# Kernel optimization log

Measured on AMD Instinct MI355X. Metric: run time of the kernel, lower is better.

## Reference

```python
import jax, jax.numpy as jnp
import numpy as np

EPS = 1e-8  # torch F.cosine_similarity default eps


def setup_inputs() -> dict:
    key = jax.random.key(0)
    k1, k2 = jax.random.split(key)
    xs_pad = jax.random.normal(k1, (8, 4096, 512), dtype=jnp.float32)
    spk_emb = jax.random.normal(k2, (8, 256, 512), dtype=jnp.float32)
    return {"xs_pad": xs_pad, "spk_emb": spk_emb}


def reference(xs_pad, spk_emb):
    # Faithful to F.cosine_similarity(x.unsqueeze(2), y.unsqueeze(1), dim=-1):
    #   dot(x, y) / (max(||x||, eps) * max(||y||, eps))
    # Implemented as L2-normalize then a batched GEMM -> (B, T, S), avoiding
    # the (B, T, S, D) broadcast intermediate.
    x_norm = jnp.maximum(jnp.linalg.norm(xs_pad, axis=-1, keepdims=True), EPS)
    y_norm = jnp.maximum(jnp.linalg.norm(spk_emb, axis=-1, keepdims=True), EPS)
    xn = xs_pad / x_norm          # (B, T, D)
    yn = spk_emb / y_norm         # (B, S, D)
    scores = jnp.einsum('btd,bsd->bts', xn, yn)  # (B, T, S)
    return scores
```

## Files before the change

### kernel.cpp

```cpp
#include <hip/hip_runtime.h>
#include <hip/hip_bf16.h>

#define BB 8
#define TT 4096
#define SS 256
#define DD 512

typedef __attribute__((ext_vector_type(8))) short short8;
typedef __attribute__((ext_vector_type(4))) float floatx4;
typedef __attribute__((ext_vector_type(4))) int intx4;

__device__ inline int pk2(float a, float b) {
  __hip_bfloat162 h = __float22bfloat162_rn(make_float2(a, b));
  int r;
  __builtin_memcpy(&r, &h, 4);
  return r;
}

__device__ inline short8 cvt8(float4 f0, float4 f1) {
  intx4 p;
  p[0] = pk2(f0.x, f0.y);
  p[1] = pk2(f0.z, f0.w);
  p[2] = pk2(f1.x, f1.y);
  p[3] = pk2(f1.z, f1.w);
  return __builtin_bit_cast(short8, p);
}

__global__ __launch_bounds__(256) void cos_packB_kernel(
    const float* __restrict__ spk, short* __restrict__ bp) {
  const int idx = blockIdx.x;
  const int b = idx >> 3;
  const int tn = (idx >> 2) & 1;
  const int kh = idx & 3;
  const int tid = threadIdx.x;
  short* dst = bp + (size_t)idx * 2048 * 8;
#pragma unroll
  for (int j = 0; j < 8; j++) {
    int u = j * 256 + tid;
    int row = u >> 4;
    int kblk = (u & 15) ^ (row & 15);
    const float* src =
        spk + ((size_t)(b * SS + tn * 128 + row)) * DD + kh * 128 + kblk * 8;
    float4 f0 = *(const float4*)src;
    float4 f1 = *(const float4*)(src + 4);
    short8 o = cvt8(f0, f1);
    *(short8*)(dst + (size_t)u * 8) = o;
  }
}

__global__ __launch_bounds__(256) void cos_fused_kernel(
    const float* __restrict__ xs, const short* __restrict__ bp,
    float* __restrict__ out) {
  __shared__ float sA[128 * 64];
  __shared__ short sB[128 * 128];
  __shared__ float scX[128];
  __shared__ float scY[128];

  const int tid = threadIdx.x;
  const int wave = tid >> 6;
  const int lane = tid & 63;
  const int tn = blockIdx.x;
  const int tm = blockIdx.y;
  const int b = blockIdx.z;

  const float* Abase = xs + ((size_t)b * TT + tm * 128) * DD;
  const short* Bbase = bp + ((size_t)(b * 2 + tn) * 4) * 2048 * 8;

  floatx4 acc[4][4];
#pragma unroll
  for (int i = 0; i < 4; i++)
#pragma unroll
    for (int j = 0; j < 4; j++) acc[i][j] = (floatx4){0.f, 0.f, 0.f, 0.f};
  floatx4 accG[4];
#pragma unroll
  for (int i = 0; i < 4; i++) accG[i] = (floatx4){0.f, 0.f, 0.f, 0.f};

  const int wm = wave >> 1;
  const int wn = wave & 1;
  const int quad = lane >> 4;
  const int l15 = lane & 15;
  const bool gramA = (wm == wn);

  int aoff[8];
#pragma unroll
  for (int j = 0; j < 8; j++) {
    int s = j * 256 + tid;
    int row = s >> 4;
    int blk = (s & 15) ^ (row & 15);
    aoff[j] = row * DD + blk * 4;
  }

  for (int kt = 0; kt < DD / 64; ++kt) {
    if ((kt & 1) == 0) {
      const short* gB = Bbase + (size_t)(kt >> 1) * 2048 * 8;
#pragma unroll
      for (int j = 0; j < 8; j++) {
        __builtin_amdgcn_global_load_lds(
            (const __attribute__((address_space(1))) unsigned int*)(gB +
                (size_t)(j * 256 + wave * 64 + lane) * 8),
            (__attribute__((address_space(3))) unsigned int*)(sB +
                (size_t)(j * 256 + wave * 64) * 8),
            16, 0, 0);
      }
    }
#pragma unroll
    for (int j = 0; j < 8; j++) {
      __builtin_amdgcn_global_load_lds(
          (const __attribute__((address_space(1))) unsigned int*)(Abase +
              aoff[j] + kt * 64),
          (__attribute__((address_space(3))) unsigned int*)(sA +
              (j * 256 + wave * 64) * 4),
          16, 0, 0);
    }
    __syncthreads();

#pragma unroll
    for (int ks = 0; ks < 2; ks++) {
      short8 af[4], bfr[4];
      const int b0s = ks * 8 + quad * 2;
      const int bslot = (kt & 1) * 8 + ks * 4 + quad;
#pragma unroll
      for (int im = 0; im < 4; im++) {
        int row = wm * 64 + im * 16 + l15;
        int s0 = b0s ^ (row & 15);
        int s1 = (b0s + 1) ^ (row & 15);
        float4 f0 = *(const float4*)(sA + row * 64 + s0 * 4);
        float4 f1 = *(const float4*)(sA + row * 64 + s1 * 4);
        af[im] = cvt8(f0, f1);
      }
#pragma unroll
      for (int in = 0; in < 4; in++) {
        int row = wn * 64 + in * 16 + l15;
        int s = bslot ^ (row & 15);
        bfr[in] = *(const short8*)(sB + row * 128 + s * 8);
      }
#pragma unroll
      for (int im = 0; im < 4; im++)
#pragma unroll
        for (int in = 0; in < 4; in++)
          acc[im][in] = __builtin_amdgcn_mfma_f32_16x16x32_bf16(
              af[im], bfr[in], acc[im][in], 0, 0, 0);
      if (gramA) {
#pragma unroll
        for (int im = 0; im < 4; im++)
          accG[im] = __builtin_amdgcn_mfma_f32_16x16x32_bf16(
              af[im], af[im], accG[im], 0, 0, 0);
      } else {
#pragma unroll
        for (int in = 0; in < 4; in++)
          accG[in] = __builtin_amdgcn_mfma_f32_16x16x32_bf16(
              bfr[in], bfr[in], accG[in], 0, 0, 0);
      }
    }
    __syncthreads();
  }

  if (quad == (l15 >> 2)) {
#pragma unroll
    for (int i = 0; i < 4; i++) {
      float inv = 1.0f / fmaxf(sqrtf(accG[i][l15 & 3]), 1e-8f);
      if (gramA)
        scX[wm * 64 + i * 16 + l15] = inv;
      else
        scY[wn * 64 + i * 16 + l15] = inv;
    }
  }
  __syncthreads();

  float* Obase = out + ((size_t)b * TT + tm * 128) * SS + tn * 128;
#pragma unroll
  for (int im = 0; im < 4; im++) {
#pragma unroll
    for (int in = 0; in < 4; in++) {
      int col = wn * 64 + in * 16 + l15;
      float yv = scY[col];
#pragma unroll
      for (int r = 0; r < 4; r++) {
        int row = wm * 64 + im * 16 + quad * 4 + r;
        Obase[row * SS + col] = acc[im][in][r] * scX[row] * yv;
      }
    }
  }
}

extern "C" void kernel_launch(void* const* d_in, const int* in_sizes, int n_in,
                              void* d_out, int out_size, void* d_ws,
                              size_t ws_size, hipStream_t stream) {
  const float* xs = (const float*)d_in[0];
  const float* spk = (const float*)d_in[1];
  float* out = (float*)d_out;
  short* bp = (short*)d_ws;

  hipLaunchKernelGGL(cos_packB_kernel, dim3(64), dim3(256), 0, stream, spk,
                     bp);
  hipLaunchKernelGGL(cos_fused_kernel, dim3(SS / 128, TT / 128, BB), dim3(256),
                     0, stream, xs, bp, out);
}
```

Before: 116.1 us.

## Widen output tile to full S=256 so each block reads its A rows once

Each block now covers all 256 speaker columns instead of 128. Grid shrinks from 2x32x8 to 32x8, and the B pack kernel writes a layout of 256 columns per K-quarter. This removes the duplicated fp32 A loads and the repeated bf16 conversion and gram accumulation for A, which the two N-tiles previously each did. In exchange each block needs about twice the accumulator registers and 64KB of LDS for B. The grid falls to 256 blocks, which may hurt occupancy and latency hiding.

```diff
diff --git a/kernel.cpp b/kernel.cpp
--- a/kernel.cpp
+++ b/kernel.cpp
@@ -29,18 +29,17 @@
 __global__ __launch_bounds__(256) void cos_packB_kernel(
     const float* __restrict__ spk, short* __restrict__ bp) {
   const int idx = blockIdx.x;
-  const int b = idx >> 3;
-  const int tn = (idx >> 2) & 1;
+  const int b = idx >> 2;
   const int kh = idx & 3;
   const int tid = threadIdx.x;
-  short* dst = bp + (size_t)idx * 2048 * 8;
+  short* dst = bp + (size_t)idx * 4096 * 8;
 #pragma unroll
-  for (int j = 0; j < 8; j++) {
+  for (int j = 0; j < 16; j++) {
     int u = j * 256 + tid;
-    int row = u >> 4;
-    int kblk = (u & 15) ^ (row & 15);
+    int col = u >> 4;
+    int kblk = (u & 15) ^ (col & 15);
     const float* src =
-        spk + ((size_t)(b * SS + tn * 128 + row)) * DD + kh * 128 + kblk * 8;
+        spk + ((size_t)(b * SS + col)) * DD + kh * 128 + kblk * 8;
     float4 f0 = *(const float4*)src;
     float4 f1 = *(const float4*)(src + 4);
     short8 o = cvt8(f0, f1);
@@ -52,28 +51,27 @@
     const float* __restrict__ xs, const short* __restrict__ bp,
     float* __restrict__ out) {
   __shared__ float sA[128 * 64];
-  __shared__ short sB[128 * 128];
+  __shared__ short sB[256 * 128];
   __shared__ float scX[128];
-  __shared__ float scY[128];
+  __shared__ float scY[256];
 
   const int tid = threadIdx.x;
   const int wave = tid >> 6;
   const int lane = tid & 63;
-  const int tn = blockIdx.x;
-  const int tm = blockIdx.y;
-  const int b = blockIdx.z;
+  const int tm = blockIdx.x;
+  const int b = blockIdx.y;
 
   const float* Abase = xs + ((size_t)b * TT + tm * 128) * DD;
-  const short* Bbase = bp + ((size_t)(b * 2 + tn) * 4) * 2048 * 8;
+  const short* Bregions = bp + (size_t)(b * 4) * 4096 * 8;
 
-  floatx4 acc[4][4];
+  floatx4 acc[4][8];
 #pragma unroll
   for (int i = 0; i < 4; i++)
 #pragma unroll
-    for (int j = 0; j < 4; j++) acc[i][j] = (floatx4){0.f, 0.f, 0.f, 0.f};
-  floatx4 accG[4];
+    for (int j = 0; j < 8; j++) acc[i][j] = (floatx4){0.f, 0.f, 0.f, 0.f};
+  floatx4 accG[8];
 #pragma unroll
-  for (int i = 0; i < 4; i++) accG[i] = (floatx4){0.f, 0.f, 0.f, 0.f};
+  for (int i = 0; i < 8; i++) accG[i] = (floatx4){0.f, 0.f, 0.f, 0.f};
 
   const int wm = wave >> 1;
   const int wn = wave & 1;
@@ -92,9 +90,9 @@
 
   for (int kt = 0; kt < DD / 64; ++kt) {
     if ((kt & 1) == 0) {
-      const short* gB = Bbase + (size_t)(kt >> 1) * 2048 * 8;
+      const short* gB = Bregions + (size_t)(kt >> 1) * 4096 * 8;
 #pragma unroll
-      for (int j = 0; j < 8; j++) {
+      for (int j = 0; j < 16; j++) {
         __builtin_amdgcn_global_load_lds(
             (const __attribute__((address_space(1))) unsigned int*)(gB +
                 (size_t)(j * 256 + wave * 64 + lane) * 8),
@@ -116,7 +114,7 @@
 
 #pragma unroll
     for (int ks = 0; ks < 2; ks++) {
-      short8 af[4], bfr[4];
+      short8 af[4], bfr[8];
       const int b0s = ks * 8 + quad * 2;
       const int bslot = (kt & 1) * 8 + ks * 4 + quad;
 #pragma unroll
@@ -129,15 +127,15 @@
         af[im] = cvt8(f0, f1);
       }
 #pragma unroll
-      for (int in = 0; in < 4; in++) {
-        int row = wn * 64 + in * 16 + l15;
-        int s = bslot ^ (row & 15);
-        bfr[in] = *(const short8*)(sB + row * 128 + s * 8);
+      for (int in = 0; in < 8; in++) {
+        int col = wn * 128 + in * 16 + l15;
+        int s = bslot ^ (col & 15);
+        bfr[in] = *(const short8*)(sB + col * 128 + s * 8);
       }
 #pragma unroll
       for (int im = 0; im < 4; im++)
 #pragma unroll
-        for (int in = 0; in < 4; in++)
+        for (int in = 0; in < 8; in++)
           acc[im][in] = __builtin_amdgcn_mfma_f32_16x16x32_bf16(
               af[im], bfr[in], acc[im][in], 0, 0, 0);
       if (gramA) {
@@ -147,7 +145,7 @@
               af[im], af[im], accG[im], 0, 0, 0);
       } else {
 #pragma unroll
-        for (int in = 0; in < 4; in++)
+        for (int in = 0; in < 8; in++)
           accG[in] = __builtin_amdgcn_mfma_f32_16x16x32_bf16(
               bfr[in], bfr[in], accG[in], 0, 0, 0);
       }
@@ -156,23 +154,26 @@
   }
 
   if (quad == (l15 >> 2)) {
+    if (gramA) {
 #pragma unroll
-    for (int i = 0; i < 4; i++) {
-      float inv = 1.0f / fmaxf(sqrtf(accG[i][l15 & 3]), 1e-8f);
-      if (gramA)
-        scX[wm * 64 + i * 16 + l15] = inv;
-      else
-        scY[wn * 64 + i * 16 + l15] = inv;
+      for (int i = 0; i < 4; i++)
+        scX[wm * 64 + i * 16 + l15] =
+            1.0f / fmaxf(sqrtf(accG[i][l15 & 3]), 1e-8f);
+    } else {
+#pragma unroll
+      for (int i = 0; i < 8; i++)
+        scY[wn * 128 + i * 16 + l15] =
+            1.0f / fmaxf(sqrtf(accG[i][l15 & 3]), 1e-8f);
     }
   }
   __syncthreads();
 
-  float* Obase = out + ((size_t)b * TT + tm * 128) * SS + tn * 128;
+  float* Obase = out + ((size_t)b * TT + tm * 128) * SS;
 #pragma unroll
   for (int im = 0; im < 4; im++) {
 #pragma unroll
-    for (int in = 0; in < 4; in++) {
-      int col = wn * 64 + in * 16 + l15;
+    for (int in = 0; in < 8; in++) {
+      int col = wn * 128 + in * 16 + l15;
       float yv = scY[col];
 #pragma unroll
       for (int r = 0; r < 4; r++) {
@@ -191,8 +192,8 @@
   float* out = (float*)d_out;
   short* bp = (short*)d_ws;
 
-  hipLaunchKernelGGL(cos_packB_kernel, dim3(64), dim3(256), 0, stream, spk,
+  hipLaunchKernelGGL(cos_packB_kernel, dim3(32), dim3(256), 0, stream, spk,
                      bp);
-  hipLaunchKernelGGL(cos_fused_kernel, dim3(SS / 128, TT / 128, BB), dim3(256),
-                     0, stream, xs, bp, out);
+  hipLaunchKernelGGL(cos_fused_kernel, dim3(TT / 128, BB), dim3(256), 0,
+                     stream, xs, bp, out);
 }
```

Measured after the change: 119.4 us. 2.9% more time.
